# Performance work log

Hardware: AMD Instinct MI355X
Metric: run time of the kernel (lower is better)

The kernel has to match this reference:

```python
import jax, jax.numpy as jnp
import numpy as np

H = 16       # num_attention_heads
HKV = 4      # num_key_value_heads
D = 128      # head_dim
CHUNK = 64   # input_chunk_size
RBS = 64     # retrieval_block_size


def setup_inputs() -> dict:
    key = jax.random.key(0)
    ks = jax.random.split(key, 9)
    B, S, HID = 1, 2048, 2048
    RLEN = 2048  # retrieval_block_num * RBS = (S // CHUNK) * RBS
    inv = 0.02
    return {
        "hidden_states": jax.random.normal(ks[0], (B, S, HID), jnp.float32),
        "cos": jax.random.uniform(ks[1], (B, S, D), jnp.float32),
        "sin": jax.random.uniform(ks[2], (B, S, D), jnp.float32),
        "retrieval_k": jax.random.normal(ks[3], (B, HKV, RLEN, D), jnp.float32),
        "retrieval_v": jax.random.normal(ks[4], (B, HKV, RLEN, D), jnp.float32),
        "Wq": jax.random.normal(ks[5], (HID, H * D), jnp.float32) * inv,
        "Wk": jax.random.normal(ks[6], (HID, HKV * D), jnp.float32) * inv,
        "Wv": jax.random.normal(ks[7], (HID, HKV * D), jnp.float32) * inv,
        "Wo": jax.random.normal(ks[8], (H * D, HID), jnp.float32) * inv,
    }


def _rope(x, cos, sin):
    # x: [B, h, S, D]; cos/sin: [B, S, D] (HF apply_rotary_pos_emb, unsqueeze head dim)
    c = cos[:, None, :, :]
    s = sin[:, None, :, :]
    x1, x2 = jnp.split(x, 2, axis=-1)
    rot = jnp.concatenate([-x2, x1], axis=-1)
    return x * c + rot * s


def reference(hidden_states, cos, sin, retrieval_k, retrieval_v, Wq, Wk, Wv, Wo):
    B, S, HID = hidden_states.shape
    G = H // HKV
    scale = D ** -0.5

    q = (hidden_states @ Wq).reshape(B, S, H, D).transpose(0, 2, 1, 3)    # [B,H,S,D]
    k = (hidden_states @ Wk).reshape(B, S, HKV, D).transpose(0, 2, 1, 3)  # [B,HKV,S,D]
    v = (hidden_states @ Wv).reshape(B, S, HKV, D).transpose(0, 2, 1, 3)

    q = _rope(q, cos, sin)
    k = _rope(k, cos, sin)

    # GQA: expand kv heads
    k_full = jnp.repeat(k, G, axis=1)  # [B,H,S,D]
    v_full = jnp.repeat(v, G, axis=1)

    # ---- causal part over input keys ----
    s1 = jnp.einsum('bhqd,bhkd->bhqk', q, k_full) * scale
    causal = jnp.tril(jnp.ones((S, S), bool))
    s1 = jnp.where(causal[None, None], s1, -jnp.inf)

    # ---- retrieval part: chunk c attends retrieval block (c-1) only ----
    C = S // CHUNK
    R = retrieval_k.shape[2] // RBS
    rK = retrieval_k.reshape(B, HKV, R, RBS, D)
    rV = retrieval_v.reshape(B, HKV, R, RBS, D)
    blk_idx = jnp.clip(jnp.arange(C) - 1, 0, R - 1)          # chunk 0 masked below
    rK_sel = jnp.repeat(rK[:, :, blk_idx], G, axis=1)        # [B,H,C,RBS,D]
    rV_sel = jnp.repeat(rV[:, :, blk_idx], G, axis=1)
    qc = q.reshape(B, H, C, CHUNK, D)
    s2 = jnp.einsum('bhcqd,bhckd->bhcqk', qc, rK_sel) * scale
    valid = (jnp.arange(C) >= 1)[None, None, :, None, None]
    s2 = jnp.where(valid, s2, -jnp.inf)

    # ---- joint (numerically stable) softmax over causal + retrieval keys ----
    m1 = jnp.max(s1, axis=-1)                                # [B,H,S]
    m2 = jnp.max(s2, axis=-1).reshape(B, H, S)               # -inf for chunk 0
    m = jnp.maximum(m1, m2)
    e1 = jnp.exp(s1 - m[..., None])
    e2 = jnp.exp(s2 - m.reshape(B, H, C, CHUNK)[..., None])
    denom = e1.sum(-1) + e2.sum(-1).reshape(B, H, S)         # [B,H,S]
    o1 = jnp.einsum('bhqk,bhkd->bhqd', e1, v_full)
    o2 = jnp.einsum('bhcqk,bhckd->bhcqd', e2, rV_sel).reshape(B, H, S, D)
    attn = (o1 + o2) / denom[..., None]                      # [B,H,S,D]

    out = attn.transpose(0, 2, 1, 3).reshape(B, S, H * D)
    return out @ Wo
```

## Files before the change

kernel.cpp:

```cpp
#include <hip/hip_runtime.h>
#include <stdint.h>

#define H_    16
#define HKV_  4
#define D_    128
#define S_    2048
#define HID_  2048
#define RLEN_ 2048

typedef unsigned short u16;
typedef __attribute__((ext_vector_type(4))) float f32x4;
typedef __attribute__((ext_vector_type(16))) float f32x16;
typedef __attribute__((ext_vector_type(8))) __bf16 bf16x8;
typedef __attribute__((ext_vector_type(4))) unsigned short u16x4;
typedef __attribute__((ext_vector_type(8))) unsigned short u16x8;
typedef __attribute__((ext_vector_type(2))) unsigned int u32x2;

__device__ __forceinline__ u16 f2bf(float f) {
  union { float f; unsigned u; } v; v.f = f;
  unsigned r = v.u + 0x7FFFu + ((v.u >> 16) & 1u);
  return (u16)(r >> 16);
}
__device__ __forceinline__ float bf2f(u16 h) {
  union { unsigned u; float f; } v; v.u = ((unsigned)h) << 16;
  return v.f;
}
__device__ __forceinline__ float lo2f(unsigned w) {
  union { unsigned u; float f; } v; v.u = w << 16; return v.f;
}
__device__ __forceinline__ float hi2f(unsigned w) {
  union { unsigned u; float f; } v; v.u = w & 0xFFFF0000u; return v.f;
}
__device__ __forceinline__ float exp2v(float x) {
  float r; asm("v_exp_f32 %0, %1" : "=v"(r) : "v"(x)); return r;
}
__device__ __forceinline__ unsigned cvtpk(float lo, float hi) {
  unsigned r; asm("v_cvt_pk_bf16_f32 %0, %1, %2" : "=v"(r) : "v"(lo), "v"(hi)); return r;
}
__device__ __forceinline__ void pl32swap(unsigned &a, unsigned &b) {
  u32x2 r = __builtin_amdgcn_permlane32_swap(a, b, false, false);
  a = r.x; b = r.y;
}
__device__ __forceinline__ float xhalf_max(float v) {
  unsigned a = __float_as_uint(v), b = a;
  pl32swap(a, b);
  return fmaxf(__uint_as_float(a), __uint_as_float(b));
}
__device__ __forceinline__ float xhalf_add(float v) {
  unsigned a = __float_as_uint(v), b = a;
  pl32swap(a, b);
  return __uint_as_float(a) + __uint_as_float(b);
}
__device__ __forceinline__ void drain_then_sync() {
  asm volatile("s_waitcnt vmcnt(0) lgkmcnt(0)" ::: "memory");
  __syncthreads();
}

#define GLL(srcp, ldsp) \
  __builtin_amdgcn_global_load_lds((const __attribute__((address_space(1))) unsigned int*)(srcp), \
                                   (__attribute__((address_space(3))) unsigned int*)(ldsp), 16, 0, 0)

__global__ void k_cvt(const float* __restrict__ in, u16* __restrict__ out, int n4) {
  int i = blockIdx.x * 256 + threadIdx.x;
  if (i >= n4) return;
  float4 v = ((const float4*)in)[i];
  u16x4 o;
  o.x = f2bf(v.x); o.y = f2bf(v.y); o.z = f2bf(v.z); o.w = f2bf(v.w);
  ((u16x4*)out)[i] = o;
}

__global__ void k_transw_qkv(const float* __restrict__ Wq, const float* __restrict__ Wk,
                             const float* __restrict__ Wv, u16* __restrict__ wtq) {
  __shared__ float tile[32][33];
  const int bid = blockIdx.x;
  const float* in; u16* out; int N, bx, by;
  if (bid < 4096)      { in = Wq; out = wtq;                          N = 2048; bx = (bid & 63) * 32;        by = (bid >> 6) * 32; }
  else if (bid < 5120) { in = Wk; out = wtq + (size_t)2048 * 2048;    N = 512;  bx = ((bid - 4096) & 15) * 32; by = ((bid - 4096) >> 4) * 32; }
  else                 { in = Wv; out = wtq + (size_t)2560 * 2048;    N = 512;  bx = ((bid - 5120) & 15) * 32; by = ((bid - 5120) >> 4) * 32; }
  const int K = 2048;
  int tx = threadIdx.x, ty = threadIdx.y;
#pragma unroll
  for (int i = 0; i < 32; i += 8)
    tile[ty + i][tx] = in[(size_t)(by + ty + i) * N + bx + tx];
  __syncthreads();
#pragma unroll
  for (int i = 0; i < 32; i += 8)
    out[(size_t)(bx + ty + i) * K + by + tx] = f2bf(tile[tx][ty + i]);
}

__global__ void k_transw(const float* __restrict__ in, u16* __restrict__ out, int K, int N) {
  __shared__ float tile[32][33];
  int bx = blockIdx.x * 32, by = blockIdx.y * 32;
  int tx = threadIdx.x, ty = threadIdx.y;
#pragma unroll
  for (int i = 0; i < 32; i += 8)
    tile[ty + i][tx] = in[(size_t)(by + ty + i) * N + bx + tx];
  __syncthreads();
#pragma unroll
  for (int i = 0; i < 32; i += 8)
    out[(size_t)(bx + ty + i) * K + by + tx] = f2bf(tile[tx][ty + i]);
}

__global__ __launch_bounds__(256) void k_gemm(const u16* __restrict__ A, const u16* __restrict__ Bt,
                                              u16* __restrict__ Cb, int M, int N, int K,
                                              int Kpart, int Krem) {
  __shared__ __attribute__((aligned(16))) u16 As[128 * 32];
  __shared__ __attribute__((aligned(16))) u16 Bs[128 * 32];
  const int bm = blockIdx.y * 128, bn = blockIdx.x * 128;
  const int kz0 = blockIdx.z * Kpart;
  const int kz1 = kz0 + Kpart + ((blockIdx.z == gridDim.z - 1) ? Krem : 0);
  u16* C = Cb + (size_t)blockIdx.z * M * N;
  const int tid = threadIdx.x, wave = tid >> 6, lane = tid & 63;
  const int wr = wave >> 1, wc = wave & 1;
  const int l15 = lane & 15, lhi = lane >> 4;
  f32x4 acc[4][4] = {};
  const u16* pA  = A  + (size_t)(bm + (tid >> 2)) * K + (tid & 3) * 8;
  const u16* pA2 = A  + (size_t)(bm + 64 + (tid >> 2)) * K + (tid & 3) * 8;
  const u16* pB  = Bt + (size_t)(bn + (tid >> 2)) * K + (tid & 3) * 8;
  const u16* pB2 = Bt + (size_t)(bn + 64 + (tid >> 2)) * K + (tid & 3) * 8;

  for (int k0 = kz0; k0 < kz1; k0 += 32) {
    __syncthreads();
    GLL(pA + k0,  As + wave * 512);
    GLL(pA2 + k0, As + 2048 + wave * 512);
    GLL(pB + k0,  Bs + wave * 512);
    GLL(pB2 + k0, Bs + 2048 + wave * 512);
    __syncthreads();
    bf16x8 af[4], bfr[4];
#pragma unroll
    for (int m = 0; m < 4; m++)
      af[m] = *(const bf16x8*)(As + (wr * 64 + m * 16 + l15) * 32 + lhi * 8);
#pragma unroll
    for (int n = 0; n < 4; n++)
      bfr[n] = *(const bf16x8*)(Bs + (wc * 64 + n * 16 + l15) * 32 + lhi * 8);
#pragma unroll
    for (int m = 0; m < 4; m++)
#pragma unroll
      for (int n = 0; n < 4; n++)
        acc[m][n] = __builtin_amdgcn_mfma_f32_16x16x32_bf16(af[m], bfr[n], acc[m][n], 0, 0, 0);
  }
  const int r0 = bm + wr * 64, c0 = bn + wc * 64;
#pragma unroll
  for (int m = 0; m < 4; m++)
#pragma unroll
    for (int n = 0; n < 4; n++) {
      int r = r0 + m * 16 + lhi * 4, cc = c0 + n * 16 + l15;
#pragma unroll
      for (int j = 0; j < 4; j++)
        C[(size_t)(r + j) * N + cc] = f2bf(acc[m][n][j]);
    }
}

__global__ void k_comb4(const u16* __restrict__ c0, float* __restrict__ out, int n8) {
  int i = blockIdx.x * 256 + threadIdx.x;
  if (i >= n8) return;
  const size_t zs = (size_t)2048 * 2048 / 8;
  u16x8 a = ((const u16x8*)c0)[i];
  u16x8 b = ((const u16x8*)c0)[i + zs];
  u16x8 cc = ((const u16x8*)c0)[i + 2 * zs];
  u16x8 d = ((const u16x8*)c0)[i + 3 * zs];
  float4 o0, o1;
  o0.x = (bf2f(a[0]) + bf2f(b[0])) + (bf2f(cc[0]) + bf2f(d[0]));
  o0.y = (bf2f(a[1]) + bf2f(b[1])) + (bf2f(cc[1]) + bf2f(d[1]));
  o0.z = (bf2f(a[2]) + bf2f(b[2])) + (bf2f(cc[2]) + bf2f(d[2]));
  o0.w = (bf2f(a[3]) + bf2f(b[3])) + (bf2f(cc[3]) + bf2f(d[3]));
  o1.x = (bf2f(a[4]) + bf2f(b[4])) + (bf2f(cc[4]) + bf2f(d[4]));
  o1.y = (bf2f(a[5]) + bf2f(b[5])) + (bf2f(cc[5]) + bf2f(d[5]));
  o1.z = (bf2f(a[6]) + bf2f(b[6])) + (bf2f(cc[6]) + bf2f(d[6]));
  o1.w = (bf2f(a[7]) + bf2f(b[7])) + (bf2f(cc[7]) + bf2f(d[7]));
  ((float4*)out)[i * 2]     = o0;
  ((float4*)out)[i * 2 + 1] = o1;
}

__global__ void k_ropeq(const u16* __restrict__ qp0, const float* __restrict__ cs,
                        const float* __restrict__ sn, u16* __restrict__ Q) {
  const u16* qp1 = qp0 + (size_t)2048 * 3072;
  const u16* qp2 = qp0 + (size_t)2 * 2048 * 3072;
  int tid = threadIdx.x;
  int idx = blockIdx.x * 4 + (tid >> 6);
  int d = tid & 63;
  int h = idx >> 11, s = idx & (S_ - 1);
  size_t base = (size_t)s * 3072 + h * 128;
  float x1 = bf2f(qp0[base + d]) + bf2f(qp1[base + d]) + bf2f(qp2[base + d]);
  float x2 = bf2f(qp0[base + d + 64]) + bf2f(qp1[base + d + 64]) + bf2f(qp2[base + d + 64]);
  float c1 = cs[s * D_ + d], s1v = sn[s * D_ + d];
  float c2 = cs[s * D_ + d + 64], s2v = sn[s * D_ + d + 64];
  const float sc = 0.12751744422f;
  u16* o = Q + ((size_t)h * S_ + s) * D_;
  o[d]      = f2bf((x1 * c1 - x2 * s1v) * sc);
  o[d + 64] = f2bf((x2 * c2 + x1 * s2v) * sc);
}

__global__ void k_ropekv(const u16* __restrict__ qp0, const float* __restrict__ cs,
                         const float* __restrict__ sn, u16* __restrict__ Ksw,
                         u16* __restrict__ Vts) {
  const u16* qp1 = qp0 + (size_t)2048 * 3072;
  const u16* qp2 = qp0 + (size_t)2 * 2048 * 3072;
  int tid = threadIdx.x;
  int idx = blockIdx.x * 4 + (tid >> 6);
  int d = tid & 63;
  int kv = idx >> 11, s = idx & (S_ - 1);
  size_t kb = (size_t)s * 3072 + 2048 + kv * 128;
  size_t vb = kb + 512;
  float x1 = bf2f(qp0[kb + d]) + bf2f(qp1[kb + d]) + bf2f(qp2[kb + d]);
  float x2 = bf2f(qp0[kb + d + 64]) + bf2f(qp1[kb + d + 64]) + bf2f(qp2[kb + d + 64]);
  float v1 = bf2f(qp0[vb + d]) + bf2f(qp1[vb + d]) + bf2f(qp2[vb + d]);
  float v2 = bf2f(qp0[vb + d + 64]) + bf2f(qp1[vb + d + 64]) + bf2f(qp2[vb + d + 64]);
  float c1 = cs[s * D_ + d], s1v = sn[s * D_ + d];
  float c2 = cs[s * D_ + d + 64], s2v = sn[s * D_ + d + 64];
  u16* ko = Ksw + ((size_t)kv * S_ + s) * D_;
  int sw = (s & 7) << 3;
  ko[d ^ sw]        = f2bf(x1 * c1 - x2 * s1v);
  ko[(d + 64) ^ sw] = f2bf(x2 * c2 + x1 * s2v);
  u16* vo = Vts + (size_t)kv * D_ * S_;
  int sc64 = s & ~63, sl = s & 63;
  vo[(size_t)d * S_        + sc64 + (sl ^ ((d & 7) << 3))]        = f2bf(v1);
  vo[(size_t)(d + 64) * S_ + sc64 + (sl ^ (((d + 64) & 7) << 3))] = f2bf(v2);
}

__global__ void k_retr(const float* __restrict__ rk, const float* __restrict__ rv,
                       u16* __restrict__ Krs, u16* __restrict__ Vtrs) {
  int tid = threadIdx.x;
  int idx = blockIdx.x * 2 + (tid >> 7);
  int d = tid & 127;
  int kv = idx >> 11, r = idx & (RLEN_ - 1);
  size_t base = ((size_t)kv * RLEN_ + r) * D_;
  Krs[base + (d ^ ((r & 7) << 3))] = f2bf(rk[base + d]);
  int rc = r & ~63, rl = r & 63;
  Vtrs[((size_t)kv * D_ + d) * RLEN_ + rc + (rl ^ ((d & 7) << 3))] = f2bf(rv[base + d]);
}

__global__ __launch_bounds__(256, 3) void k_attn(
    const u16* __restrict__ Q, const u16* __restrict__ Ksw, const u16* __restrict__ Vts,
    const u16* __restrict__ Krs, const u16* __restrict__ Vtrs,
    u16* __restrict__ Opart, float* __restrict__ Ml) {
  __shared__ __attribute__((aligned(16))) char smem[32768];
  u16* Kl = (u16*)smem;
  u16* Vl = (u16*)(smem + 16384);

  const int e = 83 - blockIdx.x, h = blockIdx.y, kvh = h >> 2;
  int c, part, np;
  if (e < 7)       { c = e;               part = 0;           np = 1; }
  else if (e < 23) { c = 7 + ((e - 7) >> 1);  part = (e - 7) & 1;  np = 2; }
  else if (e < 47) { c = 15 + (e - 23) / 3;   part = (e - 23) % 3; np = 3; }
  else if (e < 79) { c = 23 + ((e - 47) >> 2); part = (e - 47) & 3; np = 4; }
  else             { c = 31;              part = e - 79;      np = 5; }
  const int nt = (c == 0) ? 1 : (c + 2);
  const int t0 = (part * nt) / np, t1 = ((part + 1) * nt) / np;
  const int bp = h * 84 + e;

  const int tid = threadIdx.x, wave = tid >> 6, lane = tid & 63;
  const int qs = wave & 1, kp = wave >> 1;
  const int l31 = lane & 31, hf = lane >> 5;
  const int qrow = c * 64 + qs * 32 + l31;

  bf16x8 qf[8];
  {
    const u16* qp = Q + ((size_t)h * S_ + qrow) * D_ + hf * 8;
#pragma unroll
    for (int m = 0; m < 8; m++) qf[m] = *(const bf16x8*)(qp + m * 16);
  }
  float mq = -1e30f, lq = 0.f;
  f32x16 accO[4] = {};

  const int kgo = (tid >> 4) * 128 + (tid & 15) * 8;
  const int vgo = (tid >> 3) * 2048 + (tid & 7) * 8;
  u16* const kdst = Kl + wave * 512;
  u16* const vdst = Vl + wave * 512;

  const int cm1 = (c >= 1) ? (c - 1) : 0;
  const u16* krb = Krs + (size_t)kvh * RLEN_ * D_ + (size_t)cm1 * 64 * D_;
  const u16* vrb = Vtrs + (size_t)kvh * D_ * RLEN_ + cm1 * 64;
  const u16* kst = Ksw + (size_t)kvh * S_ * D_ + (size_t)t0 * 64 * D_;
  const u16* vst = Vts + (size_t)kvh * D_ * S_ + t0 * 64;
  int ts = t0;

#pragma unroll
  for (int p = 0; p < 4; p++) GLL(kst + p * 2048 + kgo, kdst + p * 2048);
#pragma unroll
  for (int p = 0; p < 4; p++) GLL(vst + p * 65536 + vgo, vdst + p * 2048);
  ts = t0 + 1;
  if (ts == c + 1) { kst = krb; vst = vrb; } else { kst += 64 * D_; vst += 64; }
  drain_then_sync();

  for (int t = t0; t < t1; t++) {
    const bool pf = (t + 1 < t1);
    f32x16 sacc = {};
    {
      const char* Kbuf = (const char*)Kl;
#pragma unroll
      for (int m = 0; m < 8; m++) {
        int by = ((kp * 32 + l31) << 8) + ((m * 32 + hf * 16) ^ ((l31 & 7) << 4));
        bf16x8 kf = *(const bf16x8*)(Kbuf + by);
        sacc = __builtin_amdgcn_mfma_f32_32x32x16_bf16(kf, qf[m], sacc, 0, 0, 0);
      }
    }
    drain_then_sync();
    if (pf) {
#pragma unroll
      for (int p = 0; p < 4; p++) GLL(kst + p * 2048 + kgo, kdst + p * 2048);
    }
    if (t == c) {
      const int koffm = (kp - qs) * 32;
#pragma unroll
      for (int r = 0; r < 16; r++) {
        int kloc = (r & 3) + 8 * (r >> 2) + 4 * hf + koffm;
        if (kloc > l31) sacc[r] = -1e30f;
      }
    }
    float tmax = sacc[0];
#pragma unroll
    for (int r = 1; r < 16; r++) tmax = fmaxf(tmax, sacc[r]);
    tmax = xhalf_max(tmax);
    if (!__all(tmax - mq <= 11.5f)) {
      float mn = fmaxf(mq, tmax);
      float f = exp2v(mq - mn);
      mq = mn; lq *= f;
#pragma unroll
      for (int dt = 0; dt < 4; dt++)
#pragma unroll
        for (int r = 0; r < 16; r++) accO[dt][r] *= f;
    }
    float ps = 0.f;
#pragma unroll
    for (int r = 0; r < 16; r++) {
      float p = exp2v(sacc[r] - mq);
      sacc[r] = p; ps += p;
    }
    lq += xhalf_add(ps);
    unsigned W[8];
#pragma unroll
    for (int g = 0; g < 4; g++) {
      W[2 * g]     = cvtpk(sacc[4 * g],     sacc[4 * g + 1]);
      W[2 * g + 1] = cvtpk(sacc[4 * g + 2], sacc[4 * g + 3]);
    }
    const char* Vbuf = (const char*)Vl;
    __builtin_amdgcn_s_setprio(1);
#pragma unroll
    for (int st = 0; st < 2; st++) {
      unsigned x0 = W[4 * st], y0 = W[4 * st + 2];
      unsigned x1 = W[4 * st + 1], y1 = W[4 * st + 3];
      pl32swap(x0, y0);
      pl32swap(x1, y1);
      union { unsigned u[4]; bf16x8 v; } pfr;
      pfr.u[0] = x0; pfr.u[1] = x1; pfr.u[2] = y0; pfr.u[3] = y1;
#pragma unroll
      for (int dt = 0; dt < 4; dt++) {
        int vby = ((dt * 32 + l31) << 7) + ((kp * 64 + st * 32 + hf * 16) ^ ((l31 & 7) << 4));
        bf16x8 vf = *(const bf16x8*)(Vbuf + vby);
        accO[dt] = __builtin_amdgcn_mfma_f32_32x32x16_bf16(vf, pfr.v, accO[dt], 0, 0, 0);
      }
    }
    __builtin_amdgcn_s_setprio(0);
    drain_then_sync();
    if (pf) {
#pragma unroll
      for (int p = 0; p < 4; p++) GLL(vst + p * 65536 + vgo, vdst + p * 2048);
      ts++;
      if (ts == c + 1) { kst = krb; vst = vrb; } else { kst += 64 * D_; vst += 64; }
    }
  }

  unsigned* mrg = (unsigned*)smem;
  const int mbase = (qs * 64 + lane) * 36;
  if (kp == 1) {
#pragma unroll
    for (int dt = 0; dt < 4; dt++)
#pragma unroll
      for (int k2 = 0; k2 < 8; k2++)
        mrg[mbase + dt * 8 + k2] = cvtpk(accO[dt][2 * k2], accO[dt][2 * k2 + 1]);
    mrg[mbase + 32] = __float_as_uint(mq);
    mrg[mbase + 33] = __float_as_uint(lq);
  }
  drain_then_sync();
  if (kp == 0) {
    float m1 = __uint_as_float(mrg[mbase + 32]);
    float l1 = __uint_as_float(mrg[mbase + 33]);
    float mm = fmaxf(mq, m1);
    float w0 = exp2v(mq - mm), w1 = exp2v(m1 - mm);
    float ll = w0 * lq + w1 * l1;
    u16* op = Opart + (size_t)bp * 8192 + (size_t)(qs * 32 + l31) * 128;
#pragma unroll
    for (int dt = 0; dt < 4; dt++)
#pragma unroll
      for (int j = 0; j < 4; j++) {
        u16x4 o;
#pragma unroll
        for (int b = 0; b < 4; b++) {
          int r = 4 * j + b;
          unsigned pw = mrg[mbase + dt * 8 + (r >> 1)];
          float pv = (r & 1) ? hi2f(pw) : lo2f(pw);
          o[b] = f2bf(w0 * accO[dt][r] + w1 * pv);
        }
        *(u16x4*)(op + dt * 32 + j * 8 + hf * 4) = o;
      }
    if (hf == 0) {
      Ml[(size_t)bp * 128 + qs * 32 + l31]      = mm;
      Ml[(size_t)bp * 128 + 64 + qs * 32 + l31] = ll;
    }
  }
}

__global__ __launch_bounds__(256) void k_combine(const u16* __restrict__ Opart,
                                                 const float* __restrict__ Ml,
                                                 u16* __restrict__ attn) {
  const int c = blockIdx.x, h = blockIdx.y;
  const int t = threadIdx.x;
  const int q = t >> 2, d0 = (t & 3) * 32;
  int base, np;
  if (c < 7)       { base = c;                 np = 1; }
  else if (c < 15) { base = 7 + 2 * (c - 7);   np = 2; }
  else if (c < 23) { base = 23 + 3 * (c - 15); np = 3; }
  else if (c < 31) { base = 47 + 4 * (c - 23); np = 4; }
  else             { base = 79;                np = 5; }
  const size_t pb = (size_t)h * 84 + base;

  float m = -1e30f;
  for (int p = 0; p < np; p++) m = fmaxf(m, Ml[(pb + p) * 128 + q]);
  float l = 0.f;
  float N[32];
#pragma unroll
  for (int i = 0; i < 32; i++) N[i] = 0.f;
  for (int p = 0; p < np; p++) {
    const float mp = Ml[(pb + p) * 128 + q];
    const float lp = Ml[(pb + p) * 128 + 64 + q];
    const float w = exp2v(mp - m);
    l += w * lp;
    const u16* op = Opart + (pb + p) * 8192 + q * 128 + d0;
#pragma unroll
    for (int i = 0; i < 4; i++) {
      u16x8 v = ((const u16x8*)op)[i];
#pragma unroll
      for (int ee = 0; ee < 8; ee++) N[i * 8 + ee] += w * bf2f(v[ee]);
    }
  }
  const float inv = 1.f / l;
  u16* dst = attn + (size_t)(c * 64 + q) * (H_ * D_) + h * 128 + d0;
#pragma unroll
  for (int i = 0; i < 4; i++) {
    u16x8 o;
#pragma unroll
    for (int ee = 0; ee < 8; ee++) o[ee] = f2bf(N[i * 8 + ee] * inv);
    ((u16x8*)dst)[i] = o;
  }
}

extern "C" void kernel_launch(void* const* d_in, const int* in_sizes, int n_in,
                              void* d_out, int out_size, void* d_ws, size_t ws_size,
                              hipStream_t stream) {
  const float* hs = (const float*)d_in[0];
  const float* cs = (const float*)d_in[1];
  const float* sn = (const float*)d_in[2];
  const float* rk = (const float*)d_in[3];
  const float* rv = (const float*)d_in[4];
  const float* Wq = (const float*)d_in[5];
  const float* Wk = (const float*)d_in[6];
  const float* Wv = (const float*)d_in[7];
  const float* Wo = (const float*)d_in[8];
  float* out = (float*)d_out;
  char* ws = (char*)d_ws;
  if (ws_size < (size_t)(56u << 20)) return;

  u16* hsb  = (u16*)(ws);
  u16* wtq  = (u16*)(ws + (8u << 20));
  u16* qkvP = (u16*)(ws + (20u << 20));
  u16* Qr   = (u16*)(ws);
  u16* Ks   = (u16*)(ws + (8u << 20));
  u16* Vts  = (u16*)(ws + (10u << 20));
  u16* Krs  = (u16*)(ws + (12u << 20));
  u16* Vtrs = (u16*)(ws + (14u << 20));
  u16* wto  = (u16*)(ws + (16u << 20));
  u16* Opart= (u16*)(ws + (24u << 20));
  float* Ml = (float*)(ws + (45u << 20));
  u16* attn = (u16*)(ws);
  u16* Cp   = (u16*)(ws + (24u << 20));

  dim3 tb(32, 8);
  k_cvt<<<4096, 256, 0, stream>>>(hs, hsb, 1048576);
  k_transw_qkv<<<6144, tb, 0, stream>>>(Wq, Wk, Wv, wtq);
  k_gemm<<<dim3(24, 16, 3), 256, 0, stream>>>(hsb, wtq, qkvP, 2048, 3072, 2048, 672, 32);
  k_ropeq<<<8192, 256, 0, stream>>>(qkvP, cs, sn, Qr);
  k_ropekv<<<2048, 256, 0, stream>>>(qkvP, cs, sn, Ks, Vts);
  k_retr<<<4096, 256, 0, stream>>>(rk, rv, Krs, Vtrs);
  k_transw<<<dim3(64, 64), tb, 0, stream>>>(Wo, wto, 2048, 2048);
  k_attn<<<dim3(84, 16), 256, 0, stream>>>(Qr, Ks, Vts, Krs, Vtrs, Opart, Ml);
  k_combine<<<dim3(32, 16), 256, 0, stream>>>(Opart, Ml, attn);
  k_gemm<<<dim3(16, 16, 4), 256, 0, stream>>>(attn, wto, Cp, 2048, 2048, 2048, 512, 0);
  k_comb4<<<2048, 256, 0, stream>>>(Cp, out, 524288);
}
```

Measured before the change: 179.0 us.

## Double-buffer GEMM LDS tiles and halve split-K partitions

```diff
diff --git a/kernel.cpp b/kernel.cpp
--- a/kernel.cpp
+++ b/kernel.cpp
@@ -104,8 +104,8 @@
 __global__ __launch_bounds__(256) void k_gemm(const u16* __restrict__ A, const u16* __restrict__ Bt,
                                               u16* __restrict__ Cb, int M, int N, int K,
                                               int Kpart, int Krem) {
-  __shared__ __attribute__((aligned(16))) u16 As[128 * 32];
-  __shared__ __attribute__((aligned(16))) u16 Bs[128 * 32];
+  __shared__ __attribute__((aligned(16))) u16 As[2][128 * 32];
+  __shared__ __attribute__((aligned(16))) u16 Bs[2][128 * 32];
   const int bm = blockIdx.y * 128, bn = blockIdx.x * 128;
   const int kz0 = blockIdx.z * Kpart;
   const int kz1 = kz0 + Kpart + ((blockIdx.z == gridDim.z - 1) ? Krem : 0);
@@ -113,31 +113,42 @@
   const int tid = threadIdx.x, wave = tid >> 6, lane = tid & 63;
   const int wr = wave >> 1, wc = wave & 1;
   const int l15 = lane & 15, lhi = lane >> 4;
+  const int so = wave * 512;
   f32x4 acc[4][4] = {};
   const u16* pA  = A  + (size_t)(bm + (tid >> 2)) * K + (tid & 3) * 8;
   const u16* pA2 = A  + (size_t)(bm + 64 + (tid >> 2)) * K + (tid & 3) * 8;
   const u16* pB  = Bt + (size_t)(bn + (tid >> 2)) * K + (tid & 3) * 8;
   const u16* pB2 = Bt + (size_t)(bn + 64 + (tid >> 2)) * K + (tid & 3) * 8;
 
+  GLL(pA + kz0,  &As[0][so]);
+  GLL(pA2 + kz0, &As[0][2048 + so]);
+  GLL(pB + kz0,  &Bs[0][so]);
+  GLL(pB2 + kz0, &Bs[0][2048 + so]);
+  drain_then_sync();
+
+  int buf = 0;
   for (int k0 = kz0; k0 < kz1; k0 += 32) {
-    __syncthreads();
-    GLL(pA + k0,  As + wave * 512);
-    GLL(pA2 + k0, As + 2048 + wave * 512);
-    GLL(pB + k0,  Bs + wave * 512);
-    GLL(pB2 + k0, Bs + 2048 + wave * 512);
-    __syncthreads();
+    const int nb = buf ^ 1;
+    if (k0 + 32 < kz1) {
+      GLL(pA + k0 + 32,  &As[nb][so]);
+      GLL(pA2 + k0 + 32, &As[nb][2048 + so]);
+      GLL(pB + k0 + 32,  &Bs[nb][so]);
+      GLL(pB2 + k0 + 32, &Bs[nb][2048 + so]);
+    }
     bf16x8 af[4], bfr[4];
 #pragma unroll
     for (int m = 0; m < 4; m++)
-      af[m] = *(const bf16x8*)(As + (wr * 64 + m * 16 + l15) * 32 + lhi * 8);
+      af[m] = *(const bf16x8*)(&As[buf][(wr * 64 + m * 16 + l15) * 32 + lhi * 8]);
 #pragma unroll
     for (int n = 0; n < 4; n++)
-      bfr[n] = *(const bf16x8*)(Bs + (wc * 64 + n * 16 + l15) * 32 + lhi * 8);
+      bfr[n] = *(const bf16x8*)(&Bs[buf][(wc * 64 + n * 16 + l15) * 32 + lhi * 8]);
 #pragma unroll
     for (int m = 0; m < 4; m++)
 #pragma unroll
       for (int n = 0; n < 4; n++)
         acc[m][n] = __builtin_amdgcn_mfma_f32_16x16x32_bf16(af[m], bfr[n], acc[m][n], 0, 0, 0);
+    drain_then_sync();
+    buf = nb;
   }
   const int r0 = bm + wr * 64, c0 = bn + wc * 64;
 #pragma unroll
@@ -151,23 +162,17 @@
     }
 }
 
-__global__ void k_comb4(const u16* __restrict__ c0, float* __restrict__ out, int n8) {
+__global__ void k_comb2(const u16* __restrict__ c0, const u16* __restrict__ c1,
+                        float* __restrict__ out, int n8) {
   int i = blockIdx.x * 256 + threadIdx.x;
   if (i >= n8) return;
-  const size_t zs = (size_t)2048 * 2048 / 8;
   u16x8 a = ((const u16x8*)c0)[i];
-  u16x8 b = ((const u16x8*)c0)[i + zs];
-  u16x8 cc = ((const u16x8*)c0)[i + 2 * zs];
-  u16x8 d = ((const u16x8*)c0)[i + 3 * zs];
+  u16x8 b = ((const u16x8*)c1)[i];
   float4 o0, o1;
-  o0.x = (bf2f(a[0]) + bf2f(b[0])) + (bf2f(cc[0]) + bf2f(d[0]));
-  o0.y = (bf2f(a[1]) + bf2f(b[1])) + (bf2f(cc[1]) + bf2f(d[1]));
-  o0.z = (bf2f(a[2]) + bf2f(b[2])) + (bf2f(cc[2]) + bf2f(d[2]));
-  o0.w = (bf2f(a[3]) + bf2f(b[3])) + (bf2f(cc[3]) + bf2f(d[3]));
-  o1.x = (bf2f(a[4]) + bf2f(b[4])) + (bf2f(cc[4]) + bf2f(d[4]));
-  o1.y = (bf2f(a[5]) + bf2f(b[5])) + (bf2f(cc[5]) + bf2f(d[5]));
-  o1.z = (bf2f(a[6]) + bf2f(b[6])) + (bf2f(cc[6]) + bf2f(d[6]));
-  o1.w = (bf2f(a[7]) + bf2f(b[7])) + (bf2f(cc[7]) + bf2f(d[7]));
+  o0.x = bf2f(a[0]) + bf2f(b[0]); o0.y = bf2f(a[1]) + bf2f(b[1]);
+  o0.z = bf2f(a[2]) + bf2f(b[2]); o0.w = bf2f(a[3]) + bf2f(b[3]);
+  o1.x = bf2f(a[4]) + bf2f(b[4]); o1.y = bf2f(a[5]) + bf2f(b[5]);
+  o1.z = bf2f(a[6]) + bf2f(b[6]); o1.w = bf2f(a[7]) + bf2f(b[7]);
   ((float4*)out)[i * 2]     = o0;
   ((float4*)out)[i * 2 + 1] = o1;
 }
@@ -175,14 +180,13 @@
 __global__ void k_ropeq(const u16* __restrict__ qp0, const float* __restrict__ cs,
                         const float* __restrict__ sn, u16* __restrict__ Q) {
   const u16* qp1 = qp0 + (size_t)2048 * 3072;
-  const u16* qp2 = qp0 + (size_t)2 * 2048 * 3072;
   int tid = threadIdx.x;
   int idx = blockIdx.x * 4 + (tid >> 6);
   int d = tid & 63;
   int h = idx >> 11, s = idx & (S_ - 1);
   size_t base = (size_t)s * 3072 + h * 128;
-  float x1 = bf2f(qp0[base + d]) + bf2f(qp1[base + d]) + bf2f(qp2[base + d]);
-  float x2 = bf2f(qp0[base + d + 64]) + bf2f(qp1[base + d + 64]) + bf2f(qp2[base + d + 64]);
+  float x1 = bf2f(qp0[base + d])      + bf2f(qp1[base + d]);
+  float x2 = bf2f(qp0[base + d + 64]) + bf2f(qp1[base + d + 64]);
   float c1 = cs[s * D_ + d], s1v = sn[s * D_ + d];
   float c2 = cs[s * D_ + d + 64], s2v = sn[s * D_ + d + 64];
   const float sc = 0.12751744422f;
@@ -195,17 +199,16 @@
                          const float* __restrict__ sn, u16* __restrict__ Ksw,
                          u16* __restrict__ Vts) {
   const u16* qp1 = qp0 + (size_t)2048 * 3072;
-  const u16* qp2 = qp0 + (size_t)2 * 2048 * 3072;
   int tid = threadIdx.x;
   int idx = blockIdx.x * 4 + (tid >> 6);
   int d = tid & 63;
   int kv = idx >> 11, s = idx & (S_ - 1);
   size_t kb = (size_t)s * 3072 + 2048 + kv * 128;
   size_t vb = kb + 512;
-  float x1 = bf2f(qp0[kb + d]) + bf2f(qp1[kb + d]) + bf2f(qp2[kb + d]);
-  float x2 = bf2f(qp0[kb + d + 64]) + bf2f(qp1[kb + d + 64]) + bf2f(qp2[kb + d + 64]);
-  float v1 = bf2f(qp0[vb + d]) + bf2f(qp1[vb + d]) + bf2f(qp2[vb + d]);
-  float v2 = bf2f(qp0[vb + d + 64]) + bf2f(qp1[vb + d + 64]) + bf2f(qp2[vb + d + 64]);
+  float x1 = bf2f(qp0[kb + d])      + bf2f(qp1[kb + d]);
+  float x2 = bf2f(qp0[kb + d + 64]) + bf2f(qp1[kb + d + 64]);
+  float v1 = bf2f(qp0[vb + d])      + bf2f(qp1[vb + d]);
+  float v2 = bf2f(qp0[vb + d + 64]) + bf2f(qp1[vb + d + 64]);
   float c1 = cs[s * D_ + d], s1v = sn[s * D_ + d];
   float c2 = cs[s * D_ + d + 64], s2v = sn[s * D_ + d + 64];
   u16* ko = Ksw + ((size_t)kv * S_ + s) * D_;
@@ -464,27 +467,27 @@
   u16* hsb  = (u16*)(ws);
   u16* wtq  = (u16*)(ws + (8u << 20));
   u16* qkvP = (u16*)(ws + (20u << 20));
-  u16* Qr   = (u16*)(ws);
-  u16* Ks   = (u16*)(ws + (8u << 20));
-  u16* Vts  = (u16*)(ws + (10u << 20));
-  u16* Krs  = (u16*)(ws + (12u << 20));
-  u16* Vtrs = (u16*)(ws + (14u << 20));
-  u16* wto  = (u16*)(ws + (16u << 20));
-  u16* Opart= (u16*)(ws + (24u << 20));
-  float* Ml = (float*)(ws + (45u << 20));
+  u16* Qr   = (u16*)(ws + (44u << 20));
+  u16* Ks   = (u16*)(ws + (52u << 20));
+  u16* Vts  = (u16*)(ws + (54u << 20));
+  u16* Krs  = (u16*)(ws + (8u << 20));
+  u16* Vtrs = (u16*)(ws + (10u << 20));
+  u16* wto  = (u16*)(ws + (12u << 20));
+  u16* Opart= (u16*)(ws + (20u << 20));
+  float* Ml = (float*)(ws + (41u << 20));
   u16* attn = (u16*)(ws);
-  u16* Cp   = (u16*)(ws + (24u << 20));
+  u16* Cp   = (u16*)(ws + (20u << 20));
 
   dim3 tb(32, 8);
   k_cvt<<<4096, 256, 0, stream>>>(hs, hsb, 1048576);
   k_transw_qkv<<<6144, tb, 0, stream>>>(Wq, Wk, Wv, wtq);
-  k_gemm<<<dim3(24, 16, 3), 256, 0, stream>>>(hsb, wtq, qkvP, 2048, 3072, 2048, 672, 32);
+  k_gemm<<<dim3(24, 16, 2), 256, 0, stream>>>(hsb, wtq, qkvP, 2048, 3072, 2048, 1024, 0);
   k_ropeq<<<8192, 256, 0, stream>>>(qkvP, cs, sn, Qr);
   k_ropekv<<<2048, 256, 0, stream>>>(qkvP, cs, sn, Ks, Vts);
   k_retr<<<4096, 256, 0, stream>>>(rk, rv, Krs, Vtrs);
   k_transw<<<dim3(64, 64), tb, 0, stream>>>(Wo, wto, 2048, 2048);
   k_attn<<<dim3(84, 16), 256, 0, stream>>>(Qr, Ks, Vts, Krs, Vtrs, Opart, Ml);
   k_combine<<<dim3(32, 16), 256, 0, stream>>>(Opart, Ml, attn);
-  k_gemm<<<dim3(16, 16, 4), 256, 0, stream>>>(attn, wto, Cp, 2048, 2048, 2048, 512, 0);
-  k_comb4<<<2048, 256, 0, stream>>>(Cp, out, 524288);
-}
+  k_gemm<<<dim3(16, 16, 2), 256, 0, stream>>>(attn, wto, Cp, 2048, 2048, 2048, 1024, 0);
+  k_comb2<<<2048, 256, 0, stream>>>(Cp, Cp + (size_t)2048 * 2048, out, 524288);
+}
```

New measurement: 161.8 us. -9.6%, faster.
